# Performance work log

Hardware: AMD Instinct MI355X
Metric: run time of the kernel (lower is better)

The kernel has to match this reference:

```python
import jax, jax.numpy as jnp
import numpy as np

DIM = 512
HEADS = 8
DIM_HEAD = 64
HIDDEN = HEADS * DIM_HEAD  # 512
B, N = 16, 4096
EPS = 1e-5


def setup_inputs() -> dict:
    key = jax.random.key(0)
    k1, k2, k3 = jax.random.split(key, 3)
    x = jax.random.normal(k1, (B, DIM, N), dtype=jnp.float32)
    # Conv1d kernel-size-1 weights stored as [out_ch, in_ch]
    w_qkv = jax.random.normal(k2, (3 * HIDDEN, DIM), dtype=jnp.float32) / np.sqrt(DIM)
    w_out = jax.random.normal(k3, (DIM, HIDDEN), dtype=jnp.float32) / np.sqrt(HIDDEN)
    b_out = jnp.zeros((DIM,), dtype=jnp.float32)
    g_out = jnp.ones((DIM,), dtype=jnp.float32)  # channel LayerNorm gamma
    return {"x": x, "w_qkv": w_qkv, "w_out": w_out, "b_out": b_out, "g_out": g_out}


def reference(x, w_qkv, w_out, b_out, g_out):
    b, c, n = x.shape
    scale = DIM_HEAD ** (-0.5)
    # 1x1 conv projection to q,k,v: [b, 3*hidden, n]
    qkv = jnp.einsum('bcn,oc->bon', x, w_qkv)
    q, k, v = jnp.split(qkv, 3, axis=1)
    rs = lambda t: t.reshape(b, HEADS, DIM_HEAD, n)  # b (m d) n -> b m d n
    q, k, v = rs(q), rs(k), rs(v)
    q = jax.nn.softmax(q, axis=2) * scale  # softmax over head-dim d
    k = jax.nn.softmax(k, axis=3)          # softmax over sequence n
    # context: k v^T outer-product summed over sequence -> [b, m, d, d]
    context = jnp.einsum('bmin,bmjn->bmij', k, v)
    # apply context to queries -> [b, m, d, n]
    out = jnp.einsum('bmij,bmin->bmjn', context, q)
    out = out.reshape(b, HIDDEN, n)  # b m d n -> b (m d) n
    # output 1x1 conv with bias
    out = jnp.einsum('bcn,oc->bon', out, w_out) + b_out[None, :, None]
    # channel LayerNorm (gamma-only, biased variance over channel axis)
    mean = out.mean(axis=1, keepdims=True)
    var = out.var(axis=1, keepdims=True)
    return (out - mean) * jax.lax.rsqrt(var + EPS) * g_out[None, :, None]
```

## Files before the change

### kernel.cpp

```cpp
#include <hip/hip_runtime.h>

#define NB 16
#define CDIM 512
#define NHEAD 8
#define DHEAD 64
#define NSEQ 4096
#define O3 1536

typedef __attribute__((ext_vector_type(8))) short short8;
typedef __attribute__((ext_vector_type(4))) float f32x4;
typedef __attribute__((ext_vector_type(4))) unsigned u32x4;
typedef __attribute__((ext_vector_type(2))) unsigned u32x2;
typedef __attribute__((ext_vector_type(4))) float fvec4;

__device__ __forceinline__ float bf2f(unsigned short u){
  union { unsigned u; float f; } v; v.u = ((unsigned)u) << 16; return v.f;
}
__device__ __forceinline__ unsigned short f2bf(float f){
  union { float f; unsigned u; } v; v.f = f;
  unsigned r = v.u + 0x7fffu + ((v.u >> 16) & 1u);
  return (unsigned short)(r >> 16);
}
__device__ __forceinline__ unsigned pack2(float a, float b){
  return (unsigned)f2bf(a) | ((unsigned)f2bf(b) << 16);
}
__device__ __forceinline__ void gld_lds16(const void* g, void* l){
  __builtin_amdgcn_global_load_lds(
      (const __attribute__((address_space(1))) unsigned*)g,
      (__attribute__((address_space(3))) unsigned*)l, 16, 0, 0);
}

__global__ __launch_bounds__(256) void k_conv_w(const float* __restrict__ w,
                                                unsigned short* __restrict__ o){
  int i = (blockIdx.x*256 + threadIdx.x)*4;
  fvec4 v = *(const fvec4*)(w + i);
  u32x2 p; p[0] = pack2(v[0], v[1]); p[1] = pack2(v[2], v[3]);
  *(u32x2*)(o + i) = p;
}

__global__ __launch_bounds__(256) void k_transpose_x(const float* __restrict__ x,
                                                     unsigned short* __restrict__ xT){
  __shared__ unsigned short tile[64][65];
  int b = blockIdx.z, c0 = blockIdx.y*64, n0 = blockIdx.x*64;
  int t = threadIdx.x;
  const float* xb = x + ((size_t)b*CDIM + c0)*NSEQ + n0;
  #pragma unroll
  for (int i=0;i<4;i++){
    int idx = t + i*256;
    int r = idx>>4, c4 = (idx&15)*4;
    fvec4 v = *(const fvec4*)(xb + (size_t)r*NSEQ + c4);
    tile[r][c4]   = f2bf(v[0]);
    tile[r][c4+1] = f2bf(v[1]);
    tile[r][c4+2] = f2bf(v[2]);
    tile[r][c4+3] = f2bf(v[3]);
  }
  __syncthreads();
  unsigned short* ob = xT + ((size_t)b*NSEQ + n0)*CDIM + c0;
  #pragma unroll
  for (int i=0;i<4;i++){
    int idx = t + i*256;
    int r = idx>>4, c4 = (idx&15)*4;
    u32x2 p;
    p[0] = (unsigned)tile[c4][r]   | ((unsigned)tile[c4+1][r] << 16);
    p[1] = (unsigned)tile[c4+2][r] | ((unsigned)tile[c4+3][r] << 16);
    *(u32x2*)(ob + (size_t)r*CDIM + c4) = p;
  }
}

__global__ __launch_bounds__(256) void k_gemm_kv(const unsigned short* __restrict__ A,
                                                 const unsigned short* __restrict__ Bt,
                                                 unsigned short* __restrict__ KV){
  __shared__ unsigned short As[128*32];
  __shared__ unsigned short Bs[128*32];
  int b = blockIdx.z;
  int n0 = blockIdx.x*128, o0 = blockIdx.y*128;
  const unsigned short* Bb = Bt + (size_t)b*NSEQ*CDIM;
  unsigned short* Cb = KV + (size_t)b*1024*NSEQ;
  int t = threadIdx.x, w = t>>6, l = t&63;
  int lr = l&15, kq = (l>>4)*8;
  int wr = (w>>1)*64, wc = (w&1)*64;
  f32x4 acc[4][4];
  #pragma unroll
  for (int mi=0;mi<4;mi++)
    #pragma unroll
    for (int ni=0;ni<4;ni++) acc[mi][ni] = (f32x4){0.f,0.f,0.f,0.f};
  for (int k0=0;k0<CDIM;k0+=32){
    #pragma unroll
    for (int it=0;it<2;++it){
      int chunk = it*256 + t;
      int row = chunk>>2, kc = (chunk&3)*8;
      gld_lds16(A  + (size_t)(o0+row)*CDIM + k0 + kc, (char*)As + (size_t)chunk*16);
      gld_lds16(Bb + (size_t)(n0+row)*CDIM + k0 + kc, (char*)Bs + (size_t)chunk*16);
    }
    __syncthreads();
    short8 af[4], bfv[4];
    #pragma unroll
    for (int mi=0;mi<4;mi++) af[mi]  = *(const short8*)&As[(wr + mi*16 + lr)*32 + kq];
    #pragma unroll
    for (int ni=0;ni<4;ni++) bfv[ni] = *(const short8*)&Bs[(wc + ni*16 + lr)*32 + kq];
    #pragma unroll
    for (int mi=0;mi<4;mi++)
      #pragma unroll
      for (int ni=0;ni<4;ni++)
        acc[mi][ni] = __builtin_amdgcn_mfma_f32_16x16x32_bf16(af[mi], bfv[ni], acc[mi][ni], 0, 0, 0);
    __syncthreads();
  }
  #pragma unroll
  for (int mi=0;mi<4;mi++)
    #pragma unroll
    for (int ni=0;ni<4;ni++)
      #pragma unroll
      for (int r=0;r<4;r++){
        int row = o0 + wr + mi*16 + (l>>4)*4 + r;
        int col = n0 + wc + ni*16 + lr;
        Cb[(size_t)row*NSEQ + col] = f2bf(acc[mi][ni][r]);
      }
}

#define TS 136
__global__ __launch_bounds__(256) void k_gemm_q(const unsigned short* __restrict__ A,
                                                const unsigned short* __restrict__ Bt,
                                                unsigned short* __restrict__ qsmT){
  __shared__ unsigned short smem[64*TS];
  unsigned short* As = smem;
  unsigned short* Bs = smem + 4096;
  int b = blockIdx.z;
  int n0 = blockIdx.x*128, o0 = blockIdx.y*128;
  const unsigned short* Bb = Bt + (size_t)b*NSEQ*CDIM;
  int t = threadIdx.x, w = t>>6, l = t&63;
  int lr = l&15, kq = (l>>4)*8;
  int wr = (w>>1)*64, wc = (w&1)*64;
  f32x4 acc[4][4];
  #pragma unroll
  for (int mi=0;mi<4;mi++)
    #pragma unroll
    for (int ni=0;ni<4;ni++) acc[mi][ni] = (f32x4){0.f,0.f,0.f,0.f};
  for (int k0=0;k0<CDIM;k0+=32){
    #pragma unroll
    for (int it=0;it<2;++it){
      int chunk = it*256 + t;
      int row = chunk>>2, kc = (chunk&3)*8;
      gld_lds16(A  + (size_t)(o0+row)*CDIM + k0 + kc, (char*)As + (size_t)chunk*16);
      gld_lds16(Bb + (size_t)(n0+row)*CDIM + k0 + kc, (char*)Bs + (size_t)chunk*16);
    }
    __syncthreads();
    short8 af[4], bfv[4];
    #pragma unroll
    for (int mi=0;mi<4;mi++) af[mi]  = *(const short8*)&As[(wr + mi*16 + lr)*32 + kq];
    #pragma unroll
    for (int ni=0;ni<4;ni++) bfv[ni] = *(const short8*)&Bs[(wc + ni*16 + lr)*32 + kq];
    #pragma unroll
    for (int mi=0;mi<4;mi++)
      #pragma unroll
      for (int ni=0;ni<4;ni++)
        acc[mi][ni] = __builtin_amdgcn_mfma_f32_16x16x32_bf16(af[mi], bfv[ni], acc[mi][ni], 0, 0, 0);
    __syncthreads();
  }
  unsigned pk[4][4][2];
  #pragma unroll
  for (int ni=0;ni<4;ni++){
    float mx = -1e30f;
    #pragma unroll
    for (int mi=0;mi<4;mi++)
      #pragma unroll
      for (int r=0;r<4;r++) mx = fmaxf(mx, acc[mi][ni][r]);
    mx = fmaxf(mx, __shfl_xor(mx, 16, 64));
    mx = fmaxf(mx, __shfl_xor(mx, 32, 64));
    float s = 0.f;
    #pragma unroll
    for (int mi=0;mi<4;mi++)
      #pragma unroll
      for (int r=0;r<4;r++){
        float p = __expf(acc[mi][ni][r] - mx);
        acc[mi][ni][r] = p; s += p;
      }
    s += __shfl_xor(s, 16, 64);
    s += __shfl_xor(s, 32, 64);
    float inv = 0.125f / s;
    #pragma unroll
    for (int mi=0;mi<4;mi++){
      pk[mi][ni][0] = pack2(acc[mi][ni][0]*inv, acc[mi][ni][1]*inv);
      pk[mi][ni][1] = pack2(acc[mi][ni][2]*inv, acc[mi][ni][3]*inv);
    }
  }
  #pragma unroll
  for (int ck=0;ck<2;++ck){
    if ((w&1) == ck){
      #pragma unroll
      for (int mi=0;mi<4;mi++)
        #pragma unroll
        for (int ni=0;ni<4;ni++){
          int idx = (ni*16 + lr)*TS + wr + mi*16 + (l>>4)*4;
          u32x2 p; p[0] = pk[mi][ni][0]; p[1] = pk[mi][ni][1];
          *(u32x2*)&smem[idx] = p;
        }
    }
    __syncthreads();
    int col = t>>2, rs = (t&3)*32;
    unsigned short* dst = qsmT + ((size_t)b*NSEQ + n0 + ck*64 + col)*CDIM + o0 + rs;
    #pragma unroll
    for (int j=0;j<4;++j)
      *(u32x4*)(dst + j*8) = *(const u32x4*)&smem[col*TS + rs + j*8];
    __syncthreads();
  }
}

__global__ __launch_bounds__(256) void k_kstats(const unsigned short* __restrict__ KV,
                                                float* __restrict__ kmax, float* __restrict__ ksum){
  int w = threadIdx.x>>6, l = threadIdx.x&63;
  int idx = blockIdx.x*4 + w;
  int b = idx>>9, row = idx&511;
  const unsigned short* kp = KV + ((size_t)b*1024 + row)*NSEQ;
  u32x4 kv[8];
  #pragma unroll
  for (int it=0;it<8;++it) kv[it] = ((const u32x4*)kp)[it*64 + l];
  float mx = -1e30f;
  #pragma unroll
  for (int it=0;it<8;++it)
    #pragma unroll
    for (int c=0;c<4;++c){
      unsigned u = kv[it][c];
      mx = fmaxf(mx, fmaxf(bf2f((unsigned short)u), bf2f((unsigned short)(u>>16))));
    }
  #pragma unroll
  for (int s=1;s<64;s<<=1) mx = fmaxf(mx, __shfl_xor(mx, s, 64));
  float sm = 0.f;
  #pragma unroll
  for (int it=0;it<8;++it)
    #pragma unroll
    for (int c=0;c<4;++c){
      unsigned u = kv[it][c];
      sm += __expf(bf2f((unsigned short)u) - mx) + __expf(bf2f((unsigned short)(u>>16)) - mx);
    }
  #pragma unroll
  for (int s=1;s<64;s<<=1) sm += __shfl_xor(sm, s, 64);
  if (l == 0){ kmax[idx] = mx; ksum[idx] = sm; }
}

__global__ __launch_bounds__(256) void k_context(const unsigned short* __restrict__ KV,
                                                 const float* __restrict__ kmax,
                                                 const float* __restrict__ ksum,
                                                 float* __restrict__ ctx4){
  __shared__ unsigned short Vs[64*64];
  int m = blockIdx.x, b = blockIdx.y, ch = blockIdx.z;
  int t = threadIdx.x, w = t>>6, l = t&63;
  int lr = l&15, kq = (l>>4)*8;
  const unsigned short* kbase = KV + ((size_t)b*1024 + m*64)*NSEQ;
  const unsigned short* vbase = KV + ((size_t)b*1024 + 512 + m*64)*NSEQ;
  int irow = w*16 + lr;
  float rmax = kmax[b*512 + m*64 + irow];
  f32x4 acc[4];
  #pragma unroll
  for (int jf=0;jf<4;++jf) acc[jf] = (f32x4){0.f,0.f,0.f,0.f};
  int nbeg = ch*1024, nend = nbeg + 1024;
  for (int n0=nbeg;n0<nend;n0+=64){
    #pragma unroll
    for (int it=0;it<2;++it){
      int chunk = it*256 + t;
      int row = chunk>>3, kc = (chunk&7)*8;
      gld_lds16(vbase + (size_t)row*NSEQ + n0 + kc, (char*)Vs + (size_t)chunk*16);
    }
    __syncthreads();
    #pragma unroll
    for (int kk=0;kk<2;++kk){
      u32x4 kraw = *(const u32x4*)(kbase + (size_t)irow*NSEQ + n0 + kk*32 + kq);
      short8 af;
      #pragma unroll
      for (int c=0;c<4;++c){
        unsigned u = kraw[c];
        float f0 = __expf(bf2f((unsigned short)u) - rmax);
        float f1 = __expf(bf2f((unsigned short)(u>>16)) - rmax);
        af[c*2]   = (short)f2bf(f0);
        af[c*2+1] = (short)f2bf(f1);
      }
      #pragma unroll
      for (int jf=0;jf<4;++jf){
        short8 bv = *(const short8*)&Vs[(jf*16+lr)*64 + kk*32 + kq];
        acc[jf] = __builtin_amdgcn_mfma_f32_16x16x32_bf16(af, bv, acc[jf], 0, 0, 0);
      }
    }
    __syncthreads();
  }
  float* cb = ctx4 + (((size_t)ch*NB + b)*NHEAD + m)*4096;
  #pragma unroll
  for (int jf=0;jf<4;++jf)
    #pragma unroll
    for (int r=0;r<4;++r){
      int i = w*16 + (l>>4)*4 + r;
      int j = jf*16 + lr;
      cb[i*64 + j] = acc[jf][r] / ksum[b*512 + m*64 + i];
    }
}

__global__ __launch_bounds__(256) void k_weff(const float* __restrict__ ctx4,
                                              const float* __restrict__ wout,
                                              unsigned short* __restrict__ weff){
  __shared__ float cs[64][65];
  int m = blockIdx.x, b = blockIdx.y, z = blockIdx.z;
  int t = threadIdx.x, w = t>>6, l = t&63;
  const float* cb = ctx4 + ((size_t)b*NHEAD + m)*4096;
  const size_t chs = (size_t)NB*NHEAD*4096;
  for (int idx=t; idx<4096; idx+=256)
    cs[idx>>6][idx&63] = cb[idx] + cb[idx+chs] + cb[idx+2*chs] + cb[idx+3*chs];
  __syncthreads();
  for (int oo=0;oo<32;++oo){
    int o = z*128 + w*32 + oo;
    float acc = 0.f;
    #pragma unroll
    for (int j=0;j<64;++j) acc += wout[(size_t)o*CDIM + m*64 + j] * cs[l][j];
    weff[((size_t)b*CDIM + o)*CDIM + m*64 + l] = f2bf(acc);
  }
}

__global__ __launch_bounds__(512) void k_out_ln(const unsigned short* __restrict__ Weff,
                                                const unsigned short* __restrict__ QT,
                                                const float* __restrict__ bias,
                                                const float* __restrict__ g,
                                                float* __restrict__ out){
  __shared__ unsigned short As[512*32];
  __shared__ unsigned short Bs[128*32];
  __shared__ float lnS[128], lnS2[128];
  int b = blockIdx.y, n0 = blockIdx.x*128;
  const unsigned short* Ab = Weff + (size_t)b*CDIM*CDIM;
  const unsigned short* Bb = QT + ((size_t)b*NSEQ + n0)*CDIM;
  int t = threadIdx.x, w = t>>6, l = t&63;
  int lr = l&15, kq = (l>>4)*8;
  f32x4 acc[4][8];
  #pragma unroll
  for (int mi=0;mi<4;mi++)
    #pragma unroll
    for (int ni=0;ni<8;ni++) acc[mi][ni] = (f32x4){0.f,0.f,0.f,0.f};
  for (int k0=0;k0<CDIM;k0+=32){
    #pragma unroll
    for (int it=0;it<4;++it){
      int chunk = it*512 + t;
      int row = chunk>>2, kc = (chunk&3)*8;
      gld_lds16(Ab + (size_t)row*CDIM + k0 + kc, (char*)As + (size_t)chunk*16);
    }
    {
      int row = t>>2, kc = (t&3)*8;
      gld_lds16(Bb + (size_t)row*CDIM + k0 + kc, (char*)Bs + (size_t)t*16);
    }
    __syncthreads();
    short8 af[4], bfv[8];
    #pragma unroll
    for (int mi=0;mi<4;mi++) af[mi]  = *(const short8*)&As[(w*64 + mi*16 + lr)*32 + kq];
    #pragma unroll
    for (int ni=0;ni<8;ni++) bfv[ni] = *(const short8*)&Bs[(ni*16 + lr)*32 + kq];
    #pragma unroll
    for (int mi=0;mi<4;mi++)
      #pragma unroll
      for (int ni=0;ni<8;ni++)
        acc[mi][ni] = __builtin_amdgcn_mfma_f32_16x16x32_bf16(af[mi], bfv[ni], acc[mi][ni], 0, 0, 0);
    __syncthreads();
  }
  if (t < 128){ lnS[t] = 0.f; lnS2[t] = 0.f; }
  __syncthreads();
  float ps[8], ps2[8];
  #pragma unroll
  for (int ni=0;ni<8;ni++){ ps[ni]=0.f; ps2[ni]=0.f; }
  #pragma unroll
  for (int mi=0;mi<4;mi++)
    #pragma unroll
    for (int r=0;r<4;r++){
      int row = w*64 + mi*16 + (l>>4)*4 + r;
      float bb = bias[row];
      #pragma unroll
      for (int ni=0;ni<8;ni++){
        float v = acc[mi][ni][r] + bb;
        acc[mi][ni][r] = v;
        ps[ni] += v; ps2[ni] += v*v;
      }
    }
  #pragma unroll
  for (int ni=0;ni<8;ni++){
    ps[ni]  += __shfl_xor(ps[ni], 16, 64);  ps[ni]  += __shfl_xor(ps[ni], 32, 64);
    ps2[ni] += __shfl_xor(ps2[ni], 16, 64); ps2[ni] += __shfl_xor(ps2[ni], 32, 64);
  }
  if ((l>>4) == 0){
    #pragma unroll
    for (int ni=0;ni<8;ni++){
      atomicAdd(&lnS[ni*16+lr],  ps[ni]);
      atomicAdd(&lnS2[ni*16+lr], ps2[ni]);
    }
  }
  __syncthreads();
  if (t < 128){
    float mean = lnS[t]*(1.f/512.f);
    float var  = lnS2[t]*(1.f/512.f) - mean*mean;
    lnS[t] = mean; lnS2[t] = rsqrtf(var + 1e-5f);
  }
  __syncthreads();
  float* ob = out + (size_t)b*CDIM*NSEQ + n0;
  #pragma unroll
  for (int ni=0;ni<8;ni++){
    int col = ni*16 + lr;
    float mean = lnS[col], rstd = lnS2[col];
    #pragma unroll
    for (int mi=0;mi<4;mi++)
      #pragma unroll
      for (int r=0;r<4;r++){
        int row = w*64 + mi*16 + (l>>4)*4 + r;
        ob[(size_t)row*NSEQ + col] = (acc[mi][ni][r] - mean)*rstd*g[row];
      }
  }
}

extern "C" void kernel_launch(void* const* d_in, const int* in_sizes, int n_in,
                              void* d_out, int out_size, void* d_ws, size_t ws_size,
                              hipStream_t stream){
  const float* x     = (const float*)d_in[0];
  const float* w_qkv = (const float*)d_in[1];
  const float* w_out = (const float*)d_in[2];
  const float* b_out = (const float*)d_in[3];
  const float* g_out = (const float*)d_in[4];
  float* out = (float*)d_out;
  char* ws = (char*)d_ws;

  size_t off = 0;
  unsigned short* wq_bf = (unsigned short*)(ws + off); off += (size_t)O3*CDIM*2;
  char* xT_region = ws + off;                          off += (size_t)NB*NSEQ*CDIM*2;
  unsigned short* qkv_kv = (unsigned short*)(ws + off); off += (size_t)NB*1024*NSEQ*2;
  unsigned short* qsmT   = (unsigned short*)(ws + off); off += (size_t)NB*NSEQ*CDIM*2;
  if (off > ws_size) return;
  unsigned short* xT = (unsigned short*)xT_region;
  float* kmaxp = (float*)(xT_region);
  float* ksump = (float*)(xT_region + (64<<10));
  float* ctx4  = (float*)(xT_region + (1<<20));
  unsigned short* weff = (unsigned short*)(xT_region + (16<<20));

  k_conv_w     <<<O3*CDIM/1024, 256, 0, stream>>>(w_qkv, wq_bf);
  k_transpose_x<<<dim3(NSEQ/64, CDIM/64, NB), 256, 0, stream>>>(x, xT);
  k_gemm_kv    <<<dim3(NSEQ/128, 8, NB), 256, 0, stream>>>(wq_bf + (size_t)512*CDIM, xT, qkv_kv);
  k_gemm_q     <<<dim3(NSEQ/128, 4, NB), 256, 0, stream>>>(wq_bf, xT, qsmT);
  k_kstats     <<<NB*CDIM/4, 256, 0, stream>>>(qkv_kv, kmaxp, ksump);
  k_context    <<<dim3(NHEAD, NB, 4), 256, 0, stream>>>(qkv_kv, kmaxp, ksump, ctx4);
  k_weff       <<<dim3(NHEAD, NB, 4), 256, 0, stream>>>(ctx4, w_out, weff);
  k_out_ln     <<<dim3(NSEQ/128, NB), 512, 0, stream>>>(weff, qsmT, b_out, g_out, out);
}
```

Baseline: 380.8 us.

## Rewrite K/V projection GEMM as 256x256 tile, 8-wave, double-buffered pipelined kernel

Replaces the 128x128, single-buffered k_gemm_kv with a 512-thread kernel that computes 256x256 output tiles. It uses 128 KB of LDS double-buffered in 64-wide K chunks, with XOR swizzling to avoid bank conflicts and issues global-to-LDS loads in quarter stages interleaved with the MFMA phases. It also uses s_setprio and explicit barriers to overlap memory with compute and raise operand reuse. The cost is much higher register use (128 accumulator floats per lane) and LDS use, which limits occupancy, plus more complex synchronisation.

Measured after the change: 392.6 us. 1.03x slower.

```diff
diff --git a/kernel.cpp b/kernel.cpp
--- a/kernel.cpp
+++ b/kernel.cpp
@@ -67,52 +67,131 @@
   }
 }
 
-__global__ __launch_bounds__(256) void k_gemm_kv(const unsigned short* __restrict__ A,
-                                                 const unsigned short* __restrict__ Bt,
-                                                 unsigned short* __restrict__ KV){
-  __shared__ unsigned short As[128*32];
-  __shared__ unsigned short Bs[128*32];
-  int b = blockIdx.z;
-  int n0 = blockIdx.x*128, o0 = blockIdx.y*128;
-  const unsigned short* Bb = Bt + (size_t)b*NSEQ*CDIM;
-  unsigned short* Cb = KV + (size_t)b*1024*NSEQ;
+__global__ __launch_bounds__(512,2) void k_gemm_kv8(const unsigned short* __restrict__ A,
+                                                    const unsigned short* __restrict__ Bt,
+                                                    unsigned short* __restrict__ KV){
+  __shared__ char lds[131072];
   int t = threadIdx.x, w = t>>6, l = t&63;
   int lr = l&15, kq = (l>>4)*8;
-  int wr = (w>>1)*64, wc = (w&1)*64;
-  f32x4 acc[4][4];
-  #pragma unroll
-  for (int mi=0;mi<4;mi++)
+  int wm = w>>2, wn = w&3;
+  int n0 = blockIdx.x*256, o0 = blockIdx.y*256, b = blockIdx.z;
+  const unsigned short* Ab = A + (size_t)o0*CDIM;
+  const unsigned short* Bb = Bt + ((size_t)b*NSEQ + n0)*CDIM;
+
+  auto STAGE = [&](int h){
+    if (h >= 32) return;
+    int jh = h>>2, part = h&3;
+    char* region = lds + (((jh&1)<<16) | ((part>>1)<<15));
+    const unsigned short* g = (part < 2 ? Ab : Bb) + jh*64;
+    int halfbase = (part&1)<<14;
+    #pragma unroll
+    for (int c=0;c<2;++c){
+      int rel = halfbase + c*8192 + t*16;
+      int srel = rel ^ (((rel>>9)&3)<<5);
+      gld_lds16(g + (size_t)(srel>>7)*CDIM + ((srel&127)>>1), region + rel);
+    }
+  };
+  auto FRAG = [&](const char* region, int row, int kb)->short8{
+    int off = row*128 + kb;
+    off ^= ((off>>9)&3)<<5;
+    return *(const short8*)(region + off);
+  };
+
+  f32x4 acc[8][4];
+  #pragma unroll
+  for (int mi=0;mi<8;mi++)
     #pragma unroll
     for (int ni=0;ni<4;ni++) acc[mi][ni] = (f32x4){0.f,0.f,0.f,0.f};
-  for (int k0=0;k0<CDIM;k0+=32){
-    #pragma unroll
-    for (int it=0;it<2;++it){
-      int chunk = it*256 + t;
-      int row = chunk>>2, kc = (chunk&3)*8;
-      gld_lds16(A  + (size_t)(o0+row)*CDIM + k0 + kc, (char*)As + (size_t)chunk*16);
-      gld_lds16(Bb + (size_t)(n0+row)*CDIM + k0 + kc, (char*)Bs + (size_t)chunk*16);
-    }
-    __syncthreads();
-    short8 af[4], bfv[4];
-    #pragma unroll
-    for (int mi=0;mi<4;mi++) af[mi]  = *(const short8*)&As[(wr + mi*16 + lr)*32 + kq];
-    #pragma unroll
-    for (int ni=0;ni<4;ni++) bfv[ni] = *(const short8*)&Bs[(wc + ni*16 + lr)*32 + kq];
-    #pragma unroll
-    for (int mi=0;mi<4;mi++)
-      #pragma unroll
-      for (int ni=0;ni<4;ni++)
-        acc[mi][ni] = __builtin_amdgcn_mfma_f32_16x16x32_bf16(af[mi], bfv[ni], acc[mi][ni], 0, 0, 0);
-    __syncthreads();
-  }
-  #pragma unroll
-  for (int mi=0;mi<4;mi++)
-    #pragma unroll
-    for (int ni=0;ni<4;ni++)
-      #pragma unroll
-      for (int r=0;r<4;r++){
-        int row = o0 + wr + mi*16 + (l>>4)*4 + r;
-        int col = n0 + wc + ni*16 + lr;
+
+  #pragma unroll
+  for (int h=0;h<5;++h) STAGE(h);
+
+  for (int j=0;j<8;++j){
+    if (j==7){ asm volatile("s_waitcnt vmcnt(0)" ::: "memory"); }
+    else     { asm volatile("s_waitcnt vmcnt(2)" ::: "memory"); }
+    __builtin_amdgcn_sched_barrier(0);
+    __builtin_amdgcn_s_barrier();
+    const char* Ar = lds + ((j&1)<<16);
+    const char* Br = Ar + 32768;
+    short8 aF[4][2], bF0[2][2], bF1[2][2];
+    #pragma unroll
+    for (int mi=0;mi<4;++mi)
+      #pragma unroll
+      for (int kk=0;kk<2;++kk)
+        aF[mi][kk] = FRAG(Ar, wm*128 + mi*16 + lr, kk*64 + kq*2);
+    #pragma unroll
+    for (int ni=0;ni<2;++ni)
+      #pragma unroll
+      for (int kk=0;kk<2;++kk)
+        bF0[ni][kk] = FRAG(Br, wn*64 + ni*16 + lr, kk*64 + kq*2);
+    STAGE(4*j+5);
+    __builtin_amdgcn_s_barrier();
+    __builtin_amdgcn_s_setprio(1);
+    #pragma unroll
+    for (int mi=0;mi<4;++mi)
+      #pragma unroll
+      for (int ni=0;ni<2;++ni)
+        #pragma unroll
+        for (int kk=0;kk<2;++kk)
+          acc[mi][ni] = __builtin_amdgcn_mfma_f32_16x16x32_bf16(aF[mi][kk], bF0[ni][kk], acc[mi][ni], 0, 0, 0);
+    __builtin_amdgcn_s_setprio(0);
+    __builtin_amdgcn_s_barrier();
+    #pragma unroll
+    for (int ni=0;ni<2;++ni)
+      #pragma unroll
+      for (int kk=0;kk<2;++kk)
+        bF1[ni][kk] = FRAG(Br, wn*64 + 32 + ni*16 + lr, kk*64 + kq*2);
+    STAGE(4*j+6);
+    __builtin_amdgcn_s_barrier();
+    __builtin_amdgcn_s_setprio(1);
+    #pragma unroll
+    for (int mi=0;mi<4;++mi)
+      #pragma unroll
+      for (int ni=0;ni<2;++ni)
+        #pragma unroll
+        for (int kk=0;kk<2;++kk)
+          acc[mi][2+ni] = __builtin_amdgcn_mfma_f32_16x16x32_bf16(aF[mi][kk], bF1[ni][kk], acc[mi][2+ni], 0, 0, 0);
+    __builtin_amdgcn_s_setprio(0);
+    __builtin_amdgcn_s_barrier();
+    #pragma unroll
+    for (int mi=0;mi<4;++mi)
+      #pragma unroll
+      for (int kk=0;kk<2;++kk)
+        aF[mi][kk] = FRAG(Ar, wm*128 + 64 + mi*16 + lr, kk*64 + kq*2);
+    STAGE(4*j+7);
+    __builtin_amdgcn_s_barrier();
+    __builtin_amdgcn_s_setprio(1);
+    #pragma unroll
+    for (int mi=0;mi<4;++mi)
+      #pragma unroll
+      for (int ni=0;ni<2;++ni)
+        #pragma unroll
+        for (int kk=0;kk<2;++kk)
+          acc[4+mi][2+ni] = __builtin_amdgcn_mfma_f32_16x16x32_bf16(aF[mi][kk], bF1[ni][kk], acc[4+mi][2+ni], 0, 0, 0);
+    __builtin_amdgcn_s_setprio(0);
+    __builtin_amdgcn_s_barrier();
+    __builtin_amdgcn_sched_barrier(0);
+    STAGE(4*j+8);
+    __builtin_amdgcn_s_barrier();
+    __builtin_amdgcn_s_setprio(1);
+    #pragma unroll
+    for (int mi=0;mi<4;++mi)
+      #pragma unroll
+      for (int ni=0;ni<2;++ni)
+        #pragma unroll
+        for (int kk=0;kk<2;++kk)
+          acc[4+mi][ni] = __builtin_amdgcn_mfma_f32_16x16x32_bf16(aF[mi][kk], bF0[ni][kk], acc[4+mi][ni], 0, 0, 0);
+    __builtin_amdgcn_s_setprio(0);
+  }
+  unsigned short* Cb = KV + (size_t)b*1024*NSEQ;
+  #pragma unroll
+  for (int mi=0;mi<8;++mi)
+    #pragma unroll
+    for (int ni=0;ni<4;++ni)
+      #pragma unroll
+      for (int r=0;r<4;++r){
+        int row = o0 + wm*128 + mi*16 + (l>>4)*4 + r;
+        int col = n0 + wn*64 + ni*16 + lr;
         Cb[(size_t)row*NSEQ + col] = f2bf(acc[mi][ni][r]);
       }
 }
@@ -431,7 +510,7 @@
 
   k_conv_w     <<<O3*CDIM/1024, 256, 0, stream>>>(w_qkv, wq_bf);
   k_transpose_x<<<dim3(NSEQ/64, CDIM/64, NB), 256, 0, stream>>>(x, xT);
-  k_gemm_kv    <<<dim3(NSEQ/128, 8, NB), 256, 0, stream>>>(wq_bf + (size_t)512*CDIM, xT, qkv_kv);
+  k_gemm_kv8   <<<dim3(NSEQ/256, 4, NB), 512, 0, stream>>>(wq_bf + (size_t)512*CDIM, xT, qkv_kv);
   k_gemm_q     <<<dim3(NSEQ/128, 4, NB), 256, 0, stream>>>(wq_bf, xT, qsmT);
   k_kstats     <<<NB*CDIM/4, 256, 0, stream>>>(qkv_kv, kmaxp, ksump);
   k_context    <<<dim3(NHEAD, NB, 4), 256, 0, stream>>>(qkv_kv, kmaxp, ksump, ctx4);
```

## Fuse key softmax stats into context kernel with per-chunk online rescaling

Applied to the files above, without the earlier changes.

Removes the separate k_kstats pass that read all of K. Each context block now computes a chunk-local max of K, accumulates the exp-sum alongside the MFMA loop, and writes per-chunk max and sum. k_weff merges the four chunks with log-sum-exp rescaling before applying the 1/Z normalisation. Separately, the transpose kernel now writes 16-byte vectors instead of 8-byte ones. The cost is an extra K read inside k_context for the local max and a little more work in k_weff.

Result: no change. 379.9 us (-0.2%).

```diff
diff --git a/kernel.cpp b/kernel.cpp
--- a/kernel.cpp
+++ b/kernel.cpp
@@ -57,13 +57,14 @@
   __syncthreads();
   unsigned short* ob = xT + ((size_t)b*NSEQ + n0)*CDIM + c0;
   #pragma unroll
-  for (int i=0;i<4;i++){
-    int idx = t + i*256;
-    int r = idx>>4, c4 = (idx&15)*4;
-    u32x2 p;
-    p[0] = (unsigned)tile[c4][r]   | ((unsigned)tile[c4+1][r] << 16);
-    p[1] = (unsigned)tile[c4+2][r] | ((unsigned)tile[c4+3][r] << 16);
-    *(u32x2*)(ob + (size_t)r*CDIM + c4) = p;
+  for (int i=0;i<2;i++){
+    int chunk = t + i*256;
+    int r = chunk>>3, c8 = (chunk&7)*8;
+    u32x4 p;
+    #pragma unroll
+    for (int k=0;k<4;k++)
+      p[k] = (unsigned)tile[c8+2*k][r] | ((unsigned)tile[c8+2*k+1][r] << 16);
+    *(u32x4*)(ob + (size_t)r*CDIM + c8) = p;
   }
 }
 
@@ -205,42 +206,10 @@
   }
 }
 
-__global__ __launch_bounds__(256) void k_kstats(const unsigned short* __restrict__ KV,
-                                                float* __restrict__ kmax, float* __restrict__ ksum){
-  int w = threadIdx.x>>6, l = threadIdx.x&63;
-  int idx = blockIdx.x*4 + w;
-  int b = idx>>9, row = idx&511;
-  const unsigned short* kp = KV + ((size_t)b*1024 + row)*NSEQ;
-  u32x4 kv[8];
-  #pragma unroll
-  for (int it=0;it<8;++it) kv[it] = ((const u32x4*)kp)[it*64 + l];
-  float mx = -1e30f;
-  #pragma unroll
-  for (int it=0;it<8;++it)
-    #pragma unroll
-    for (int c=0;c<4;++c){
-      unsigned u = kv[it][c];
-      mx = fmaxf(mx, fmaxf(bf2f((unsigned short)u), bf2f((unsigned short)(u>>16))));
-    }
-  #pragma unroll
-  for (int s=1;s<64;s<<=1) mx = fmaxf(mx, __shfl_xor(mx, s, 64));
-  float sm = 0.f;
-  #pragma unroll
-  for (int it=0;it<8;++it)
-    #pragma unroll
-    for (int c=0;c<4;++c){
-      unsigned u = kv[it][c];
-      sm += __expf(bf2f((unsigned short)u) - mx) + __expf(bf2f((unsigned short)(u>>16)) - mx);
-    }
-  #pragma unroll
-  for (int s=1;s<64;s<<=1) sm += __shfl_xor(sm, s, 64);
-  if (l == 0){ kmax[idx] = mx; ksum[idx] = sm; }
-}
-
 __global__ __launch_bounds__(256) void k_context(const unsigned short* __restrict__ KV,
-                                                 const float* __restrict__ kmax,
-                                                 const float* __restrict__ ksum,
-                                                 float* __restrict__ ctx4){
+                                                 float* __restrict__ ctx4,
+                                                 float* __restrict__ maxp,
+                                                 float* __restrict__ sump){
   __shared__ unsigned short Vs[64*64];
   int m = blockIdx.x, b = blockIdx.y, ch = blockIdx.z;
   int t = threadIdx.x, w = t>>6, l = t&63;
@@ -248,12 +217,28 @@
   const unsigned short* kbase = KV + ((size_t)b*1024 + m*64)*NSEQ;
   const unsigned short* vbase = KV + ((size_t)b*1024 + 512 + m*64)*NSEQ;
   int irow = w*16 + lr;
-  float rmax = kmax[b*512 + m*64 + irow];
+  int sub = l>>4;
+  int nbeg = ch*1024;
+  float mx = -1e30f;
+  {
+    const unsigned short* kp = kbase + (size_t)irow*NSEQ + nbeg + sub*256;
+    #pragma unroll
+    for (int it=0;it<32;++it){
+      u32x4 kv4 = *(const u32x4*)(kp + it*8);
+      #pragma unroll
+      for (int c=0;c<4;++c){
+        unsigned u = kv4[c];
+        mx = fmaxf(mx, fmaxf(bf2f((unsigned short)u), bf2f((unsigned short)(u>>16))));
+      }
+    }
+    mx = fmaxf(mx, __shfl_xor(mx, 16, 64));
+    mx = fmaxf(mx, __shfl_xor(mx, 32, 64));
+  }
+  float rsum = 0.f;
   f32x4 acc[4];
   #pragma unroll
   for (int jf=0;jf<4;++jf) acc[jf] = (f32x4){0.f,0.f,0.f,0.f};
-  int nbeg = ch*1024, nend = nbeg + 1024;
-  for (int n0=nbeg;n0<nend;n0+=64){
+  for (int n0=nbeg;n0<nbeg+1024;n0+=64){
     #pragma unroll
     for (int it=0;it<2;++it){
       int chunk = it*256 + t;
@@ -268,8 +253,9 @@
       #pragma unroll
       for (int c=0;c<4;++c){
         unsigned u = kraw[c];
-        float f0 = __expf(bf2f((unsigned short)u) - rmax);
-        float f1 = __expf(bf2f((unsigned short)(u>>16)) - rmax);
+        float f0 = __expf(bf2f((unsigned short)u) - mx);
+        float f1 = __expf(bf2f((unsigned short)(u>>16)) - mx);
+        rsum += f0 + f1;
         af[c*2]   = (short)f2bf(f0);
         af[c*2+1] = (short)f2bf(f1);
       }
@@ -281,6 +267,10 @@
     }
     __syncthreads();
   }
+  rsum += __shfl_xor(rsum, 16, 64);
+  rsum += __shfl_xor(rsum, 32, 64);
+  size_t sbase = (((size_t)ch*NB + b)*NHEAD + m)*64;
+  if (sub == 0){ maxp[sbase + irow] = mx; sump[sbase + irow] = rsum; }
   float* cb = ctx4 + (((size_t)ch*NB + b)*NHEAD + m)*4096;
   #pragma unroll
   for (int jf=0;jf<4;++jf)
@@ -288,20 +278,40 @@
     for (int r=0;r<4;++r){
       int i = w*16 + (l>>4)*4 + r;
       int j = jf*16 + lr;
-      cb[i*64 + j] = acc[jf][r] / ksum[b*512 + m*64 + i];
+      cb[i*64 + j] = acc[jf][r];
     }
 }
 
 __global__ __launch_bounds__(256) void k_weff(const float* __restrict__ ctx4,
+                                              const float* __restrict__ maxp,
+                                              const float* __restrict__ sump,
                                               const float* __restrict__ wout,
                                               unsigned short* __restrict__ weff){
   __shared__ float cs[64][65];
+  __shared__ float wch[4][64];
+  __shared__ float invZ[64];
   int m = blockIdx.x, b = blockIdx.y, z = blockIdx.z;
   int t = threadIdx.x, w = t>>6, l = t&63;
+  const size_t chs = (size_t)NB*NHEAD*4096;
+  const size_t sts = (size_t)NB*NHEAD*64;
+  size_t sb = ((size_t)b*NHEAD + m)*64;
+  if (t < 64){
+    float m0 = maxp[sb + t], m1 = maxp[sb + sts + t];
+    float m2 = maxp[sb + 2*sts + t], m3 = maxp[sb + 3*sts + t];
+    float M = fmaxf(fmaxf(m0,m1), fmaxf(m2,m3));
+    float w0 = __expf(m0-M), w1 = __expf(m1-M), w2 = __expf(m2-M), w3 = __expf(m3-M);
+    float Z = sump[sb + t]*w0 + sump[sb + sts + t]*w1
+            + sump[sb + 2*sts + t]*w2 + sump[sb + 3*sts + t]*w3;
+    wch[0][t] = w0; wch[1][t] = w1; wch[2][t] = w2; wch[3][t] = w3;
+    invZ[t] = 1.f/Z;
+  }
+  __syncthreads();
   const float* cb = ctx4 + ((size_t)b*NHEAD + m)*4096;
-  const size_t chs = (size_t)NB*NHEAD*4096;
-  for (int idx=t; idx<4096; idx+=256)
-    cs[idx>>6][idx&63] = cb[idx] + cb[idx+chs] + cb[idx+2*chs] + cb[idx+3*chs];
+  for (int idx=t; idx<4096; idx+=256){
+    int i = idx>>6;
+    cs[i][idx&63] = (cb[idx]*wch[0][i] + cb[idx+chs]*wch[1][i]
+                   + cb[idx+2*chs]*wch[2][i] + cb[idx+3*chs]*wch[3][i]) * invZ[i];
+  }
   __syncthreads();
   for (int oo=0;oo<32;++oo){
     int o = z*128 + w*32 + oo;
@@ -424,17 +434,16 @@
   unsigned short* qsmT   = (unsigned short*)(ws + off); off += (size_t)NB*NSEQ*CDIM*2;
   if (off > ws_size) return;
   unsigned short* xT = (unsigned short*)xT_region;
-  float* kmaxp = (float*)(xT_region);
-  float* ksump = (float*)(xT_region + (64<<10));
-  float* ctx4  = (float*)(xT_region + (1<<20));
+  float* maxp = (float*)(xT_region);
+  float* sump = (float*)(xT_region + (256<<10));
+  float* ctx4 = (float*)(xT_region + (1<<20));
   unsigned short* weff = (unsigned short*)(xT_region + (16<<20));
 
   k_conv_w     <<<O3*CDIM/1024, 256, 0, stream>>>(w_qkv, wq_bf);
   k_transpose_x<<<dim3(NSEQ/64, CDIM/64, NB), 256, 0, stream>>>(x, xT);
   k_gemm_kv    <<<dim3(NSEQ/128, 8, NB), 256, 0, stream>>>(wq_bf + (size_t)512*CDIM, xT, qkv_kv);
   k_gemm_q     <<<dim3(NSEQ/128, 4, NB), 256, 0, stream>>>(wq_bf, xT, qsmT);
-  k_kstats     <<<NB*CDIM/4, 256, 0, stream>>>(qkv_kv, kmaxp, ksump);
-  k_context    <<<dim3(NHEAD, NB, 4), 256, 0, stream>>>(qkv_kv, kmaxp, ksump, ctx4);
-  k_weff       <<<dim3(NHEAD, NB, 4), 256, 0, stream>>>(ctx4, w_out, weff);
+  k_context    <<<dim3(NHEAD, NB, 4), 256, 0, stream>>>(qkv_kv, ctx4, maxp, sump);
+  k_weff       <<<dim3(NHEAD, NB, 4), 256, 0, stream>>>(ctx4, maxp, sump, w_out, weff);
   k_out_ln     <<<dim3(NSEQ/128, NB), 512, 0, stream>>>(weff, qsmT, b_out, g_out, out);
 }
```
